# Kernel tuning notes

Measured on AMD Instinct MI355X. Metric: run time of the kernel, lower is better.

The kernel has to match this reference:

```python
import jax, jax.numpy as jnp
import numpy as np


def setup_inputs() -> dict:
    key = jax.random.key(0)
    k1, k2, k3, k4 = jax.random.split(key, 4)
    B, M, N = 8, 4096, 4096
    return {
        "pc_src": jax.random.normal(k1, (B, 3, M), dtype=jnp.float32),
        "pc_dst": jax.random.normal(k2, (B, 3, N), dtype=jnp.float32),
        "sigma_src": jax.random.uniform(k3, (B, M), dtype=jnp.float32),
        "sigma_dst": jax.random.uniform(k4, (B, N), dtype=jnp.float32),
    }


def reference(pc_src, pc_dst, sigma_src, sigma_dst):
    # Pairwise Euclidean distance: diff[b, m, n] = ||pc_src[b,:,m] - pc_dst[b,:,n]||_2
    d = pc_src[:, :, :, None] - pc_dst[:, :, None, :]  # [B, 3, M, N]
    diff = jnp.sqrt(jnp.sum(d * d, axis=1))            # [B, M, N]

    # src -> dst
    src_dst_min_dist = jnp.min(diff, axis=2)           # [B, M]
    src_dst_I = jnp.argmin(diff, axis=2)               # [B, M]
    selected_sigma_dst = jnp.take_along_axis(sigma_dst, src_dst_I, axis=1)
    sigma_src_dst = (sigma_src + selected_sigma_dst) / 2
    forward_loss = jnp.mean(src_dst_min_dist * sigma_src_dst)

    # dst -> src
    dst_src_min_dist = jnp.min(diff, axis=1)           # [B, N]
    dst_src_I = jnp.argmin(diff, axis=1)               # [B, N]
    selected_sigma_src = jnp.take_along_axis(sigma_src, dst_src_I, axis=1)
    sigma_dst_src = (sigma_dst + selected_sigma_src) / 2
    backward_loss = jnp.mean(dst_src_min_dist * sigma_dst_src)

    return forward_loss + backward_loss
```

## Files before the change

kernel.cpp:

```cpp
#include <hip/hip_runtime.h>
#include <math.h>
#include <cfloat>

#define BLOCK 256
#define QPT 4

__global__ void chamfer_min_kernel(const float* __restrict__ pcq,
                                   const float* __restrict__ pcr,
                                   float2* __restrict__ part,
                                   int NQ, int NR, int CS, int B,
                                   float* out_zero) {
    extern __shared__ float4 lds[];
    const int b = blockIdx.y;
    const int chunk = blockIdx.z;
    const int tid = threadIdx.x;
    const int n0 = chunk * CS;

    if (out_zero && blockIdx.x == 0 && b == 0 && chunk == 0 && tid == 0)
        *out_zero = 0.0f;

    const float* rbase = pcr + (size_t)b * 3 * NR;
    for (int i = tid; i < CS; i += BLOCK) {
        float rx = rbase[n0 + i];
        float ry = rbase[NR + n0 + i];
        float rz = rbase[2 * NR + n0 + i];
        lds[i] = make_float4(-2.0f * rx, -2.0f * ry, -2.0f * rz,
                             rx * rx + ry * ry + rz * rz);
    }

    const int q0 = blockIdx.x * (BLOCK * QPT) + tid;
    const float* qbase = pcq + (size_t)b * 3 * NQ;
    float qx[QPT], qy[QPT], qz[QPT], emin[QPT];
    int imin[QPT];
#pragma unroll
    for (int j = 0; j < QPT; ++j) {
        const int q = q0 + j * BLOCK;
        qx[j] = qbase[q];
        qy[j] = qbase[NQ + q];
        qz[j] = qbase[2 * NQ + q];
        emin[j] = FLT_MAX;
        imin[j] = 0;
    }

    __syncthreads();

#pragma unroll 4
    for (int i = 0; i < CS; ++i) {
        const float4 r = lds[i];
#pragma unroll
        for (int j = 0; j < QPT; ++j) {
            float e = fmaf(qx[j], r.x, r.w);
            e = fmaf(qy[j], r.y, e);
            e = fmaf(qz[j], r.z, e);
            if (e < emin[j]) { emin[j] = e; imin[j] = i; }
        }
    }

#pragma unroll
    for (int j = 0; j < QPT; ++j) {
        const int q = q0 + j * BLOCK;
        part[((size_t)chunk * B + b) * NQ + q] =
            make_float2(emin[j], (float)(n0 + imin[j]));
    }
}

__global__ void chamfer_reduce_kernel(const float* __restrict__ pc_src,
                                      const float* __restrict__ pc_dst,
                                      const float* __restrict__ sig_src,
                                      const float* __restrict__ sig_dst,
                                      const float2* __restrict__ part0,
                                      const float2* __restrict__ part1,
                                      float* __restrict__ out,
                                      int M, int N, int B, int RC) {
    __shared__ float red[BLOCK];
    const int TT = blockIdx.x * BLOCK + threadIdx.x;
    const int dir = (TT >= B * M);
    const int t = dir ? TT - B * M : TT;

    const int NQ = dir ? N : M;
    const int NR = dir ? M : N;
    const float* pcq  = dir ? pc_dst : pc_src;
    const float* sigq = dir ? sig_dst : sig_src;
    const float* sigr = dir ? sig_src : sig_dst;
    const float2* part = dir ? part1 : part0;
    const float scale = 1.0f / (float)(B * NQ);

    const int b = t / NQ;
    const int q = t - b * NQ;

    float emin = FLT_MAX;
    float fidx = 0.0f;
    for (int c = 0; c < RC; ++c) {
        const float2 pc = part[((size_t)c * B + b) * NQ + q];
        if (pc.x < emin) { emin = pc.x; fidx = pc.y; }
    }

    const float* qbase = pcq + (size_t)b * 3 * NQ;
    const float qx = qbase[q];
    const float qy = qbase[NQ + q];
    const float qz = qbase[2 * NQ + q];
    const float d2 = fmaxf(emin + (qx * qx + qy * qy + qz * qz), 0.0f);
    const float dist = sqrtf(d2);

    const int idx = (int)fidx;
    const float s = 0.5f * (sigq[t] + sigr[(size_t)b * NR + idx]);
    red[threadIdx.x] = dist * s * scale;
    __syncthreads();

    for (int w = BLOCK / 2; w > 0; w >>= 1) {
        if (threadIdx.x < w) red[threadIdx.x] += red[threadIdx.x + w];
        __syncthreads();
    }
    if (threadIdx.x == 0) atomicAdd(out, red[0]);
}

extern "C" void kernel_launch(void* const* d_in, const int* in_sizes, int n_in,
                              void* d_out, int out_size, void* d_ws, size_t ws_size,
                              hipStream_t stream) {
    const float* pc_src  = (const float*)d_in[0];
    const float* pc_dst  = (const float*)d_in[1];
    const float* sig_src = (const float*)d_in[2];
    const float* sig_dst = (const float*)d_in[3];
    float* out = (float*)d_out;

    const int B = 8;
    const int M = in_sizes[2] / B;
    const int N = in_sizes[3] / B;
    const int NMAX = (M > N) ? M : N;

    int RC = 32;
    while (RC > 1 && 2 * (size_t)B * NMAX * RC * sizeof(float2) > ws_size) RC >>= 1;

    float2* part0 = (float2*)d_ws;
    float2* part1 = part0 + (size_t)RC * B * M;

    {
        const int CS = N / RC;
        dim3 grid(M / (BLOCK * QPT), B, RC);
        chamfer_min_kernel<<<grid, BLOCK, CS * sizeof(float4), stream>>>(
            pc_src, pc_dst, part0, M, N, CS, B, out);
    }
    {
        const int CS = M / RC;
        dim3 grid(N / (BLOCK * QPT), B, RC);
        chamfer_min_kernel<<<grid, BLOCK, CS * sizeof(float4), stream>>>(
            pc_dst, pc_src, part1, N, M, CS, B, nullptr);
    }
    {
        dim3 rgrid((B * (M + N)) / BLOCK);
        chamfer_reduce_kernel<<<rgrid, BLOCK, 0, stream>>>(
            pc_src, pc_dst, sig_src, sig_dst, part0, part1, out, M, N, B, RC);
    }
}
```

Measured before the change: 60.38 us.

## Pack distance and index into one uint key and merge both directions into one launch

The inner loop now packs the float distance bits, with the low bits replaced by the local index, into a single unsigned key and takes an unsigned min. This replaces the compare-and-two-selects with one min op. A +64 offset keeps the expanded distances positive so the uint ordering matches the float ordering. Both directions now run in one launch, with QPT raised to 8, RC to 64, launch bounds added and smaller partial records, and the reduce recomputes the exact distance from the chosen index. The cost is that truncating the low mantissa bits can pick a near-tie neighbour, and correctness needs power-of-two CS and squared distances above -64.

```diff
diff --git a/kernel.cpp b/kernel.cpp
--- a/kernel.cpp
+++ b/kernel.cpp
@@ -3,47 +3,59 @@
 #include <cfloat>
 
 #define BLOCK 256
-#define QPT 4
+#define QPT 8
 
-__global__ void chamfer_min_kernel(const float* __restrict__ pcq,
-                                   const float* __restrict__ pcr,
-                                   float2* __restrict__ part,
-                                   int NQ, int NR, int CS, int B,
-                                   float* out_zero) {
+__global__ __launch_bounds__(BLOCK, 4)
+void chamfer_min_kernel(const float* __restrict__ pc_src,
+                        const float* __restrict__ pc_dst,
+                        unsigned* __restrict__ part0,
+                        unsigned* __restrict__ part1,
+                        int M, int N, int B, int RC,
+                        float* out_zero) {
     extern __shared__ float4 lds[];
     const int b = blockIdx.y;
-    const int chunk = blockIdx.z;
+    const int zc = blockIdx.z;
+    const int dir = (zc >= RC) ? 1 : 0;
+    const int chunk = zc - dir * RC;
+
+    const int NQ = dir ? N : M;
+    const int NR = dir ? M : N;
+    const float* pcq = dir ? pc_dst : pc_src;
+    const float* pcr = dir ? pc_src : pc_dst;
+    unsigned* part = dir ? part1 : part0;
+
+    const int CS = NR / RC;
+    const int n0 = chunk * CS;
     const int tid = threadIdx.x;
-    const int n0 = chunk * CS;
 
-    if (out_zero && blockIdx.x == 0 && b == 0 && chunk == 0 && tid == 0)
+    if (out_zero && blockIdx.x == 0 && b == 0 && zc == 0 && tid == 0)
         *out_zero = 0.0f;
 
     const float* rbase = pcr + (size_t)b * 3 * NR;
     for (int i = tid; i < CS; i += BLOCK) {
-        float rx = rbase[n0 + i];
-        float ry = rbase[NR + n0 + i];
-        float rz = rbase[2 * NR + n0 + i];
+        const float rx = rbase[n0 + i];
+        const float ry = rbase[NR + n0 + i];
+        const float rz = rbase[2 * NR + n0 + i];
         lds[i] = make_float4(-2.0f * rx, -2.0f * ry, -2.0f * rz,
-                             rx * rx + ry * ry + rz * rz);
+                             fmaf(rx, rx, fmaf(ry, ry, rz * rz)) + 64.0f);
     }
 
     const int q0 = blockIdx.x * (BLOCK * QPT) + tid;
     const float* qbase = pcq + (size_t)b * 3 * NQ;
-    float qx[QPT], qy[QPT], qz[QPT], emin[QPT];
-    int imin[QPT];
+    float qx[QPT], qy[QPT], qz[QPT];
+    unsigned kmin[QPT];
 #pragma unroll
     for (int j = 0; j < QPT; ++j) {
         const int q = q0 + j * BLOCK;
         qx[j] = qbase[q];
         qy[j] = qbase[NQ + q];
         qz[j] = qbase[2 * NQ + q];
-        emin[j] = FLT_MAX;
-        imin[j] = 0;
+        kmin[j] = 0xFFFFFFFFu;
     }
 
     __syncthreads();
 
+    const unsigned mask = ~(unsigned)(CS - 1);
 #pragma unroll 4
     for (int i = 0; i < CS; ++i) {
         const float4 r = lds[i];
@@ -52,15 +64,15 @@
             float e = fmaf(qx[j], r.x, r.w);
             e = fmaf(qy[j], r.y, e);
             e = fmaf(qz[j], r.z, e);
-            if (e < emin[j]) { emin[j] = e; imin[j] = i; }
+            const unsigned key = (__float_as_uint(e) & mask) | (unsigned)i;
+            kmin[j] = (key < kmin[j]) ? key : kmin[j];
         }
     }
 
 #pragma unroll
     for (int j = 0; j < QPT; ++j) {
         const int q = q0 + j * BLOCK;
-        part[((size_t)chunk * B + b) * NQ + q] =
-            make_float2(emin[j], (float)(n0 + imin[j]));
+        part[((size_t)chunk * B + b) * NQ + q] = kmin[j];
     }
 }
 
@@ -68,8 +80,8 @@
                                       const float* __restrict__ pc_dst,
                                       const float* __restrict__ sig_src,
                                       const float* __restrict__ sig_dst,
-                                      const float2* __restrict__ part0,
-                                      const float2* __restrict__ part1,
+                                      const unsigned* __restrict__ part0,
+                                      const unsigned* __restrict__ part1,
                                       float* __restrict__ out,
                                       int M, int N, int B, int RC) {
     __shared__ float red[BLOCK];
@@ -80,30 +92,32 @@
     const int NQ = dir ? N : M;
     const int NR = dir ? M : N;
     const float* pcq  = dir ? pc_dst : pc_src;
+    const float* pcr  = dir ? pc_src : pc_dst;
     const float* sigq = dir ? sig_dst : sig_src;
     const float* sigr = dir ? sig_src : sig_dst;
-    const float2* part = dir ? part1 : part0;
+    const unsigned* part = dir ? part1 : part0;
     const float scale = 1.0f / (float)(B * NQ);
+    const int CS = NR / RC;
 
     const int b = t / NQ;
     const int q = t - b * NQ;
 
-    float emin = FLT_MAX;
-    float fidx = 0.0f;
+    unsigned kbest = 0xFFFFFFFFu;
+    int cbest = 0;
     for (int c = 0; c < RC; ++c) {
-        const float2 pc = part[((size_t)c * B + b) * NQ + q];
-        if (pc.x < emin) { emin = pc.x; fidx = pc.y; }
+        const unsigned k = part[((size_t)c * B + b) * NQ + q];
+        if (k < kbest) { kbest = k; cbest = c; }
     }
+    const int gidx = cbest * CS + (int)(kbest & (unsigned)(CS - 1));
 
     const float* qbase = pcq + (size_t)b * 3 * NQ;
-    const float qx = qbase[q];
-    const float qy = qbase[NQ + q];
-    const float qz = qbase[2 * NQ + q];
-    const float d2 = fmaxf(emin + (qx * qx + qy * qy + qz * qz), 0.0f);
-    const float dist = sqrtf(d2);
+    const float* rbase = pcr + (size_t)b * 3 * NR;
+    const float dx = qbase[q]          - rbase[gidx];
+    const float dy = qbase[NQ + q]     - rbase[NR + gidx];
+    const float dz = qbase[2 * NQ + q] - rbase[2 * NR + gidx];
+    const float dist = sqrtf(fmaf(dx, dx, fmaf(dy, dy, dz * dz)));
 
-    const int idx = (int)fidx;
-    const float s = 0.5f * (sigq[t] + sigr[(size_t)b * NR + idx]);
+    const float s = 0.5f * (sigq[t] + sigr[(size_t)b * NR + gidx]);
     red[threadIdx.x] = dist * s * scale;
     __syncthreads();
 
@@ -128,23 +142,17 @@
     const int N = in_sizes[3] / B;
     const int NMAX = (M > N) ? M : N;
 
-    int RC = 32;
-    while (RC > 1 && 2 * (size_t)B * NMAX * RC * sizeof(float2) > ws_size) RC >>= 1;
+    int RC = 64;
+    while (RC > 1 && 2 * (size_t)B * NMAX * RC * sizeof(unsigned) > ws_size) RC >>= 1;
 
-    float2* part0 = (float2*)d_ws;
-    float2* part1 = part0 + (size_t)RC * B * M;
+    unsigned* part0 = (unsigned*)d_ws;
+    unsigned* part1 = part0 + (size_t)RC * B * NMAX;
 
     {
-        const int CS = N / RC;
-        dim3 grid(M / (BLOCK * QPT), B, RC);
-        chamfer_min_kernel<<<grid, BLOCK, CS * sizeof(float4), stream>>>(
-            pc_src, pc_dst, part0, M, N, CS, B, out);
-    }
-    {
-        const int CS = M / RC;
-        dim3 grid(N / (BLOCK * QPT), B, RC);
-        chamfer_min_kernel<<<grid, BLOCK, CS * sizeof(float4), stream>>>(
-            pc_dst, pc_src, part1, N, M, CS, B, nullptr);
+        const int CSMAX = NMAX / RC;
+        dim3 grid(NMAX / (BLOCK * QPT), B, 2 * RC);
+        chamfer_min_kernel<<<grid, BLOCK, CSMAX * sizeof(float4), stream>>>(
+            pc_src, pc_dst, part0, part1, M, N, B, RC, out);
     }
     {
         dim3 rgrid((B * (M + N)) / BLOCK);
```

Result: slower. 61.90 us (+2.5%).
